# Optimization experiments

Hardware: AMD Instinct MI355X
Metric: run time of the kernel (lower is better)

Reference implementation:

```python
import jax, jax.numpy as jnp
import numpy as np

V, D, H, F, L, B, S = 32000, 1024, 16, 4096, 6, 2, 1024
DH = D // H


def setup_inputs() -> dict:
    key = jax.random.key(0)
    ks = jax.random.split(key, 12)
    n = lambda k, shape: jax.random.normal(k, shape, jnp.float32) * 0.02
    inp = {}
    inp['x'] = jax.random.randint(ks[0], (B, S), 0, V)
    # causal mask: 1 = masked (upper triangle), matches masked_fill(mask==1, -inf)
    inp['mask'] = jnp.triu(jnp.ones((S, S), jnp.int32), k=1)[None, None]
    inp['embed'] = n(ks[1], (V, D))
    inp['wq'] = n(ks[2], (L, D, D)); inp['bq'] = jnp.zeros((L, D), jnp.float32)
    inp['wk'] = n(ks[3], (L, D, D)); inp['bk'] = jnp.zeros((L, D), jnp.float32)
    inp['wv'] = n(ks[4], (L, D, D)); inp['bv'] = jnp.zeros((L, D), jnp.float32)
    inp['wo'] = n(ks[5], (L, D, D)); inp['bo'] = jnp.zeros((L, D), jnp.float32)
    inp['w1'] = n(ks[6], (L, D, F)); inp['b1'] = jnp.zeros((L, F), jnp.float32)
    inp['w2'] = n(ks[7], (L, F, D)); inp['b2'] = jnp.zeros((L, D), jnp.float32)
    inp['ln1_g'] = jnp.ones((L, D), jnp.float32); inp['ln1_b'] = jnp.zeros((L, D), jnp.float32)
    inp['ln2_g'] = jnp.ones((L, D), jnp.float32); inp['ln2_b'] = jnp.zeros((L, D), jnp.float32)
    inp['lnf_g'] = jnp.ones((D,), jnp.float32); inp['lnf_b'] = jnp.zeros((D,), jnp.float32)
    inp['proj_w'] = n(ks[8], (D, V)); inp['proj_b'] = jnp.zeros((V,), jnp.float32)
    return inp


def _layernorm(x, g, b, eps=1e-5):
    mu = jnp.mean(x, axis=-1, keepdims=True)
    var = jnp.var(x, axis=-1, keepdims=True)
    return (x - mu) * jax.lax.rsqrt(var + eps) * g + b


def _positional_encoding(s, d):
    pos = jnp.arange(s, dtype=jnp.float32)[:, None]
    div = jnp.exp(jnp.arange(0, d, 2, dtype=jnp.float32) * (-jnp.log(10000.0) / d))
    pe = jnp.zeros((s, d), jnp.float32)
    pe = pe.at[:, 0::2].set(jnp.sin(pos * div))
    pe = pe.at[:, 1::2].set(jnp.cos(pos * div))
    return pe


def reference(x, mask, embed, wq, bq, wk, bk, wv, bv, wo, bo, w1, b1, w2, b2,
              ln1_g, ln1_b, ln2_g, ln2_b, lnf_g, lnf_b, proj_w, proj_b):
    b_, s_ = x.shape
    h = embed[x] * jnp.sqrt(jnp.float32(D))          # [B,S,D]
    h = h + _positional_encoding(s_, D)[None]
    scale = 1.0 / jnp.sqrt(jnp.float32(DH))

    def layer(h, p):
        Wq, Bq, Wk, Bk, Wv, Bv, Wo, Bo, W1, B1, W2, B2, G1, Be1, G2, Be2 = p
        q = (h @ Wq + Bq).reshape(b_, s_, H, DH).transpose(0, 2, 1, 3)   # [B,H,S,Dh]
        k = (h @ Wk + Bk).reshape(b_, s_, H, DH).transpose(0, 2, 1, 3)
        v = (h @ Wv + Bv).reshape(b_, s_, H, DH).transpose(0, 2, 1, 3)
        scores = jnp.einsum('bhqd,bhkd->bhqk', q, k) * scale            # [B,H,S,S]
        scores = jnp.where(mask == 1, -jnp.inf, scores)
        attn = jax.nn.softmax(scores, axis=-1)
        ctx = jnp.einsum('bhqk,bhkd->bhqd', attn, v)
        ctx = ctx.transpose(0, 2, 1, 3).reshape(b_, s_, D) @ Wo + Bo
        h = _layernorm(h + ctx, G1, Be1)
        ffn = jax.nn.relu(h @ W1 + B1) @ W2 + B2
        h = _layernorm(h + ffn, G2, Be2)
        return h, None

    h, _ = jax.lax.scan(layer, h, (wq, bq, wk, bk, wv, bv, wo, bo,
                                   w1, b1, w2, b2, ln1_g, ln1_b, ln2_g, ln2_b))
    h = _layernorm(h, lnf_g, lnf_b)
    return h @ proj_w + proj_b                                           # [B,S,V]
```

## Files before the change

kernel.cpp:

```cpp
#include <hip/hip_runtime.h>
#include <math.h>

#define D_MODEL 1024
#define NHEADS 16
#define DHEAD 64
#define FDIM 4096
#define NLAYERS 6
#define BATCH 2
#define SEQ 1024
#define NROWS (BATCH*SEQ)
#define VOCAB 32000

typedef __attribute__((ext_vector_type(4))) float f32x4;
typedef __attribute__((ext_vector_type(4))) __bf16 bf16x4;
typedef __attribute__((ext_vector_type(8))) __bf16 bf16x8;

__device__ __forceinline__ void gll16(const void* g, void* l) {
  __builtin_amdgcn_global_load_lds(
      (const __attribute__((address_space(1))) unsigned int*)g,
      (__attribute__((address_space(3))) unsigned int*)l, 16, 0, 0);
}

__global__ __launch_bounds__(256) void transpose_w(
    const float* __restrict__ W, __bf16* __restrict__ Wt, int K, int N) {
  __shared__ __bf16 Ls[64][68];
  const size_t moff = (size_t)blockIdx.z * K * N;
  const float* Wl = W + moff;
  __bf16* Wtl = Wt + moff;
  const int n0 = blockIdx.x * 64, k0 = blockIdx.y * 64;
  const int tid = threadIdx.x;
  #pragma unroll
  for (int p = 0; p < 4; ++p) {
    int e = tid + p * 256;
    int r = e >> 4, c4 = (e & 15) * 4;
    float4 v = *(const float4*)&Wl[(size_t)(k0 + r) * N + n0 + c4];
    Ls[c4 + 0][r] = (__bf16)v.x; Ls[c4 + 1][r] = (__bf16)v.y;
    Ls[c4 + 2][r] = (__bf16)v.z; Ls[c4 + 3][r] = (__bf16)v.w;
  }
  __syncthreads();
  #pragma unroll
  for (int p = 0; p < 4; ++p) {
    int e = tid + p * 256;
    int r2 = e >> 4, c8 = (e & 15) * 4;
    bf16x4 o{Ls[r2][c8], Ls[r2][c8 + 1], Ls[r2][c8 + 2], Ls[r2][c8 + 3]};
    *(bf16x4*)&Wtl[(size_t)(n0 + r2) * K + k0 + c8] = o;
  }
}

struct GemmP {
  const __bf16* A;
  const __bf16* W[3];
  const float* B[3];
  void* C[3];
  int N, K;
};

template<int BM, int RELU, int OUTF32>
__global__ __launch_bounds__(256) void gemm_bf16(GemmP g) {
  constexpr int BK = 64;
  const __bf16* __restrict__ A = g.A;
  const __bf16* __restrict__ W = g.W[blockIdx.z];
  const float* __restrict__ bias = g.B[blockIdx.z];
  const int N = g.N, K = g.K;

  __shared__ __bf16 As[2][BM * BK];
  __shared__ __bf16 Bs[2][128 * BK];

  const int tid = threadIdx.x;
  const int lane = tid & 63, w = tid >> 6;

  const int gx = gridDim.x;
  const int nblk = gx * gridDim.y;
  const int id = blockIdx.x + blockIdx.y * gx;
  const int per = nblk >> 3;
  const int sid = (id & 7) * per + (id >> 3);
  const int row0 = (sid % gx) * BM;
  const int col0 = (sid / gx) * 128;

  const int wm = w >> 1, wn = w & 1;
  const int lr = lane & 15, rsw = lr & 7;

  constexpr int MI = BM / 32;
  f32x4 acc[MI][4] = {};

  const int swg = ((lane & 7) ^ (lane >> 3)) * 8;
  const __bf16* Ag = A + (size_t)(row0 + w * (BM / 4) + (lane >> 3)) * K + swg;
  const __bf16* Wg = W + (size_t)(col0 + w * 32 + (lane >> 3)) * K + swg;

  const int NT = K / BK;

  auto stage = [&](int buf, int t) {
    const int k0 = t * BK;
    #pragma unroll
    for (int s = 0; s < BM / 32; ++s)
      gll16(Ag + (size_t)s * 8 * K + k0, &As[buf][(w * (BM / 4) + s * 8) * BK]);
    #pragma unroll
    for (int s = 0; s < 4; ++s)
      gll16(Wg + (size_t)s * 8 * K + k0, &Bs[buf][(w * 32 + s * 8) * BK]);
  };

  stage(0, 0);
  __syncthreads();

  int cur = 0;
  for (int t = 0; t < NT; ++t) {
    if (t + 1 < NT) stage(cur ^ 1, t + 1);
    #pragma unroll
    for (int kk = 0; kk < 2; ++kk) {
      const int gsw = ((kk * 4 + (lane >> 4)) ^ rsw) * 8;
      bf16x8 af[MI], bf[4];
      #pragma unroll
      for (int i = 0; i < MI; ++i)
        af[i] = *(const bf16x8*)&As[cur][(wm * (BM / 2) + i * 16 + lr) * BK + gsw];
      #pragma unroll
      for (int j = 0; j < 4; ++j)
        bf[j] = *(const bf16x8*)&Bs[cur][(wn * 64 + j * 16 + lr) * BK + gsw];
      #pragma unroll
      for (int i = 0; i < MI; ++i)
        #pragma unroll
        for (int j = 0; j < 4; ++j)
          acc[i][j] = __builtin_amdgcn_mfma_f32_16x16x32_bf16(af[i], bf[j], acc[i][j], 0, 0, 0);
    }
    __syncthreads();
    cur ^= 1;
  }

  #pragma unroll
  for (int i = 0; i < MI; ++i) {
    #pragma unroll
    for (int j = 0; j < 4; ++j) {
      int col = col0 + wn * 64 + j * 16 + lr;
      float bb = bias[col];
      #pragma unroll
      for (int r = 0; r < 4; ++r) {
        int row = row0 + wm * (BM / 2) + i * 16 + (lane >> 4) * 4 + r;
        float v = acc[i][j][r] + bb;
        if (RELU) v = fmaxf(v, 0.0f);
        if (OUTF32) ((float*)g.C[blockIdx.z])[(size_t)row * N + col] = v;
        else ((__bf16*)g.C[blockIdx.z])[(size_t)row * N + col] = (__bf16)v;
      }
    }
  }
}

__global__ __launch_bounds__(512, 1) void gemm_256(
    const __bf16* __restrict__ A, const __bf16* __restrict__ W,
    const float* __restrict__ bias, float* __restrict__ C, int N, int K) {
  extern __shared__ __bf16 sm[];
  __bf16* As = sm;
  __bf16* Bs = sm + 2 * 256 * 64;

  const int tid = threadIdx.x;
  const int lane = tid & 63, w = tid >> 6;

  const int gx = gridDim.x;
  const int nblk = gx * gridDim.y;
  const int id = blockIdx.x + blockIdx.y * gx;
  const int per = nblk >> 3;
  const int sid = (id & 7) * per + (id >> 3);
  const int row0 = (sid % gx) * 256;
  const int col0 = (sid / gx) * 256;

  const int wr = w >> 2, wc = w & 3;
  const int lr = lane & 15;

  f32x4 acc[8][4] = {};

  const int swg = ((lane & 7) ^ (lane >> 3)) * 8;
  const __bf16* Ag = A + (size_t)(row0 + w * 32 + (lane >> 3)) * K + swg;
  const __bf16* Wg = W + (size_t)(col0 + w * 32 + (lane >> 3)) * K + swg;

  const int NT = K / 64;

  auto stage = [&](int buf, int t) {
    const int k0 = t * 64;
    #pragma unroll
    for (int s = 0; s < 4; ++s) {
      gll16(Ag + (size_t)(s * 8) * K + k0, &As[buf * 16384 + (w * 32 + s * 8) * 64]);
      gll16(Wg + (size_t)(s * 8) * K + k0, &Bs[buf * 16384 + (w * 32 + s * 8) * 64]);
    }
  };

  stage(0, 0);
  __syncthreads();

  int cur = 0;
  for (int t = 0; t < NT; ++t) {
    if (t + 1 < NT) stage(cur ^ 1, t + 1);
    #pragma unroll
    for (int kk = 0; kk < 2; ++kk) {
      bf16x8 af[8], bf[4];
      #pragma unroll
      for (int i = 0; i < 8; ++i) {
        int row = wr * 128 + i * 16 + lr;
        af[i] = *(const bf16x8*)&As[cur * 16384 + row * 64 +
                                    (((kk * 4 + (lane >> 4)) ^ (row & 7)) * 8)];
      }
      #pragma unroll
      for (int j = 0; j < 4; ++j) {
        int row = wc * 64 + j * 16 + lr;
        bf[j] = *(const bf16x8*)&Bs[cur * 16384 + row * 64 +
                                    (((kk * 4 + (lane >> 4)) ^ (row & 7)) * 8)];
      }
      #pragma unroll
      for (int i = 0; i < 8; ++i)
        #pragma unroll
        for (int j = 0; j < 4; ++j)
          acc[i][j] = __builtin_amdgcn_mfma_f32_16x16x32_bf16(af[i], bf[j], acc[i][j], 0, 0, 0);
    }
    __syncthreads();
    cur ^= 1;
  }

  #pragma unroll
  for (int i = 0; i < 8; ++i) {
    #pragma unroll
    for (int j = 0; j < 4; ++j) {
      int col = col0 + wc * 64 + j * 16 + lr;
      float bb = bias[col];
      #pragma unroll
      for (int r = 0; r < 4; ++r) {
        int row = row0 + wr * 128 + i * 16 + (lane >> 4) * 4 + r;
        C[(size_t)row * N + col] = acc[i][j][r] + bb;
      }
    }
  }
}

__global__ __launch_bounds__(256) void attn_kernel(
    const __bf16* __restrict__ Q, const __bf16* __restrict__ K,
    const __bf16* __restrict__ V, __bf16* __restrict__ O) {
  __shared__ __bf16 Ks[64 * 64];
  __shared__ __bf16 Vts[64 * 64];
  __shared__ __bf16 Psm[4][16 * 64];

  const int tid = threadIdx.x;
  const int lane = tid & 63, w = tid >> 6;
  const int q0 = blockIdx.x * 64;
  const int bh = blockIdx.y;
  const int b = bh >> 4, h = bh & 15;
  const size_t base = ((size_t)b * SEQ) * D_MODEL + (size_t)h * DHEAD;

  const int lr = lane & 15;
  const int lk = (lane >> 4) * 8;

  bf16x8 qa[2];
  {
    const __bf16* qp = Q + base + (size_t)(q0 + w * 16 + lr) * D_MODEL;
    qa[0] = *(const bf16x8*)&qp[lk];
    qa[1] = *(const bf16x8*)&qp[32 + lk];
  }

  f32x4 o_acc[4] = {};
  float m[4], l[4];
  #pragma unroll
  for (int r = 0; r < 4; ++r) { m[r] = -1e30f; l[r] = 0.0f; }

  const int nck = q0 / 64 + 1;

  for (int ck = 0; ck < nck; ++ck) {
    const int kv0 = ck * 64;
    __syncthreads();
    #pragma unroll
    for (int c = 0; c < 2; ++c) {
      int e = tid + c * 256;
      int r = e >> 3, d8 = (e & 7) * 8;
      const size_t grow = base + (size_t)(kv0 + r) * D_MODEL + d8;
      bf16x8 kv = *(const bf16x8*)&K[grow];
      *(bf16x8*)&Ks[(r * 64 + d8) ^ ((r & 7) << 3)] = kv;
      bf16x8 vv = *(const bf16x8*)&V[grow];
      #pragma unroll
      for (int j = 0; j < 8; ++j)
        Vts[((d8 + j) * 64 + r) ^ (((d8 + j) & 7) << 3)] = vv[j];
    }
    __syncthreads();

    f32x4 s_acc[4] = {};
    #pragma unroll
    for (int t = 0; t < 4; ++t) {
      int row = t * 16 + lr;
      #pragma unroll
      for (int hh = 0; hh < 2; ++hh) {
        bf16x8 kb = *(const bf16x8*)&Ks[(row * 64 + hh * 32 + lk) ^ ((row & 7) << 3)];
        s_acc[t] = __builtin_amdgcn_mfma_f32_16x16x32_bf16(qa[hh], kb, s_acc[t], 0, 0, 0);
      }
    }

    const bool diag = (ck == nck - 1);
    #pragma unroll
    for (int t = 0; t < 4; ++t) {
      int kvg = kv0 + t * 16 + lr;
      #pragma unroll
      for (int r = 0; r < 4; ++r) {
        float sv = s_acc[t][r] * 0.125f;
        if (diag) {
          int qg = q0 + w * 16 + (lane >> 4) * 4 + r;
          if (kvg > qg) sv = -1e30f;
        }
        s_acc[t][r] = sv;
      }
    }

    #pragma unroll
    for (int r = 0; r < 4; ++r) {
      float cm = fmaxf(fmaxf(s_acc[0][r], s_acc[1][r]), fmaxf(s_acc[2][r], s_acc[3][r]));
      #pragma unroll
      for (int off = 1; off < 16; off <<= 1) cm = fmaxf(cm, __shfl_xor(cm, off, 64));
      float newm = fmaxf(m[r], cm);
      float sc = __expf(m[r] - newm);
      m[r] = newm;
      float psum = 0.0f;
      #pragma unroll
      for (int t = 0; t < 4; ++t) {
        float p = __expf(s_acc[t][r] - newm);
        s_acc[t][r] = p;
        psum += p;
      }
      #pragma unroll
      for (int off = 1; off < 16; off <<= 1) psum += __shfl_xor(psum, off, 64);
      l[r] = l[r] * sc + psum;
      #pragma unroll
      for (int t = 0; t < 4; ++t) o_acc[t][r] *= sc;
    }

    #pragma unroll
    for (int t = 0; t < 4; ++t) {
      #pragma unroll
      for (int r = 0; r < 4; ++r) {
        int ql = (lane >> 4) * 4 + r;
        Psm[w][(ql * 64 + t * 16 + lr) ^ ((ql & 7) << 3)] = (__bf16)(s_acc[t][r]);
      }
    }

    bf16x8 pa[2];
    #pragma unroll
    for (int hh = 0; hh < 2; ++hh)
      pa[hh] = *(const bf16x8*)&Psm[w][(lr * 64 + hh * 32 + lk) ^ ((lr & 7) << 3)];
    #pragma unroll
    for (int t = 0; t < 4; ++t) {
      int row = t * 16 + lr;
      #pragma unroll
      for (int hh = 0; hh < 2; ++hh) {
        bf16x8 vb = *(const bf16x8*)&Vts[(row * 64 + hh * 32 + lk) ^ ((row & 7) << 3)];
        o_acc[t] = __builtin_amdgcn_mfma_f32_16x16x32_bf16(pa[hh], vb, o_acc[t], 0, 0, 0);
      }
    }
  }

  #pragma unroll
  for (int r = 0; r < 4; ++r) {
    float inv = 1.0f / l[r];
    int qg = q0 + w * 16 + (lane >> 4) * 4 + r;
    #pragma unroll
    for (int t = 0; t < 4; ++t)
      O[base + (size_t)qg * D_MODEL + t * 16 + lr] = (__bf16)(o_acc[t][r] * inv);
  }
}

template<int HASRES>
__global__ __launch_bounds__(256) void addln_kernel(
    const __bf16* __restrict__ X, const __bf16* __restrict__ Rr,
    const float* __restrict__ g, const float* __restrict__ bb,
    __bf16* __restrict__ Out) {
  const int row = blockIdx.x;
  const int tid = threadIdx.x;
  const size_t rb = (size_t)row * D_MODEL + tid * 4;
  bf16x4 xv = *(const bf16x4*)&X[rb];
  float v[4];
  float s = 0.0f, ss = 0.0f;
  if (HASRES) {
    bf16x4 rv = *(const bf16x4*)&Rr[rb];
    #pragma unroll
    for (int i = 0; i < 4; ++i) {
      v[i] = (float)xv[i] + (float)rv[i];
      s += v[i]; ss += v[i] * v[i];
    }
  } else {
    #pragma unroll
    for (int i = 0; i < 4; ++i) { v[i] = (float)xv[i]; s += v[i]; ss += v[i] * v[i]; }
  }
  #pragma unroll
  for (int off = 32; off; off >>= 1) { s += __shfl_xor(s, off, 64); ss += __shfl_xor(ss, off, 64); }
  __shared__ float red[8];
  const int lane = tid & 63, w = tid >> 6;
  if (lane == 0) { red[w] = s; red[4 + w] = ss; }
  __syncthreads();
  s = red[0] + red[1] + red[2] + red[3];
  ss = red[4] + red[5] + red[6] + red[7];
  float mean = s * (1.0f / D_MODEL);
  float var = ss * (1.0f / D_MODEL) - mean * mean;
  float rs = rsqrtf(var + 1e-5f);
  const int d0 = tid * 4;
  bf16x4 ov;
  #pragma unroll
  for (int i = 0; i < 4; ++i)
    ov[i] = (__bf16)((v[i] - mean) * rs * g[d0 + i] + bb[d0 + i]);
  *(bf16x4*)&Out[rb] = ov;
}

__global__ __launch_bounds__(256) void embed_kernel(
    const int* __restrict__ x, const float* __restrict__ embed,
    __bf16* __restrict__ H) {
  const int row = blockIdx.x;
  const int spos = row & (SEQ - 1);
  const int tok = x[row];
  const int tid = threadIdx.x;
  const int d0 = tid * 4;
  float4 e4 = *(const float4*)&embed[(size_t)tok * D_MODEL + d0];
  float ev[4] = {e4.x, e4.y, e4.z, e4.w};
  bf16x4 ov;
  #pragma unroll
  for (int i = 0; i < 4; ++i) {
    int d = d0 + i;
    float div = expf((float)(2 * (d >> 1)) * (-9.2103403719761836f / (float)D_MODEL));
    float ang = (float)spos * div;
    float pe = (d & 1) ? cosf(ang) : sinf(ang);
    ov[i] = (__bf16)(ev[i] * 32.0f + pe);
  }
  *(bf16x4*)&H[(size_t)row * D_MODEL + d0] = ov;
}

extern "C" void kernel_launch(void* const* d_in, const int* in_sizes, int n_in,
                              void* d_out, int out_size, void* d_ws, size_t ws_size,
                              hipStream_t stream) {
  const int* x = (const int*)d_in[0];
  const float* embed = (const float*)d_in[2];
  const float* wq = (const float*)d_in[3];
  const float* bq = (const float*)d_in[4];
  const float* wk = (const float*)d_in[5];
  const float* bk = (const float*)d_in[6];
  const float* wv = (const float*)d_in[7];
  const float* bv = (const float*)d_in[8];
  const float* wo = (const float*)d_in[9];
  const float* bo = (const float*)d_in[10];
  const float* w1 = (const float*)d_in[11];
  const float* b1 = (const float*)d_in[12];
  const float* w2 = (const float*)d_in[13];
  const float* b2 = (const float*)d_in[14];
  const float* ln1g = (const float*)d_in[15];
  const float* ln1b = (const float*)d_in[16];
  const float* ln2g = (const float*)d_in[17];
  const float* ln2b = (const float*)d_in[18];
  const float* lnfg = (const float*)d_in[19];
  const float* lnfb = (const float*)d_in[20];
  const float* pw = (const float*)d_in[21];
  const float* pb = (const float*)d_in[22];
  float* out = (float*)d_out;

  char* wsp = (char*)d_ws;
  size_t off = 0;
  auto alloc = [&](size_t bytes) {
    void* p = wsp + off; off = (off + bytes + 255) & ~(size_t)255; return p;
  };
  const size_t RD2 = (size_t)NROWS * D_MODEL * 2;
  __bf16* Xb   = (__bf16*)alloc(RD2);
  __bf16* Qb   = (__bf16*)alloc(RD2);
  __bf16* Kb   = (__bf16*)alloc(RD2);
  __bf16* Vb   = (__bf16*)alloc(RD2);
  __bf16* CTXb = (__bf16*)alloc(RD2);
  __bf16* Tb   = (__bf16*)alloc(RD2);
  __bf16* H1b  = (__bf16*)alloc(RD2);
  __bf16* FFb  = Qb;
  const size_t DD = (size_t)D_MODEL * D_MODEL;
  const size_t DF = (size_t)D_MODEL * FDIM;
  __bf16* wqt = (__bf16*)alloc(NLAYERS * DD * 2);
  __bf16* wkt = (__bf16*)alloc(NLAYERS * DD * 2);
  __bf16* wvt = (__bf16*)alloc(NLAYERS * DD * 2);
  __bf16* wot = (__bf16*)alloc(NLAYERS * DD * 2);
  __bf16* w1t = (__bf16*)alloc(NLAYERS * DF * 2);
  __bf16* w2t = (__bf16*)alloc(NLAYERS * DF * 2);
  __bf16* pwt = (__bf16*)alloc((size_t)D_MODEL * VOCAB * 2);

  transpose_w<<<dim3(16, 16, NLAYERS), 256, 0, stream>>>(wq, wqt, D_MODEL, D_MODEL);
  transpose_w<<<dim3(16, 16, NLAYERS), 256, 0, stream>>>(wk, wkt, D_MODEL, D_MODEL);
  transpose_w<<<dim3(16, 16, NLAYERS), 256, 0, stream>>>(wv, wvt, D_MODEL, D_MODEL);
  transpose_w<<<dim3(16, 16, NLAYERS), 256, 0, stream>>>(wo, wot, D_MODEL, D_MODEL);
  transpose_w<<<dim3(64, 16, NLAYERS), 256, 0, stream>>>(w1, w1t, D_MODEL, FDIM);
  transpose_w<<<dim3(16, 64, NLAYERS), 256, 0, stream>>>(w2, w2t, FDIM, D_MODEL);
  transpose_w<<<dim3(500, 16, 1), 256, 0, stream>>>(pw, pwt, D_MODEL, VOCAB);

  embed_kernel<<<NROWS, 256, 0, stream>>>(x, embed, Xb);

  for (int l = 0; l < NLAYERS; ++l) {
    GemmP g{};
    g.A = Xb; g.N = D_MODEL; g.K = D_MODEL;
    g.W[0] = wqt + l * DD; g.W[1] = wkt + l * DD; g.W[2] = wvt + l * DD;
    g.B[0] = bq + l * D_MODEL; g.B[1] = bk + l * D_MODEL; g.B[2] = bv + l * D_MODEL;
    g.C[0] = Qb; g.C[1] = Kb; g.C[2] = Vb;
    gemm_bf16<128, 0, 0><<<dim3(NROWS / 128, D_MODEL / 128, 3), 256, 0, stream>>>(g);

    attn_kernel<<<dim3(SEQ / 64, BATCH * NHEADS), 256, 0, stream>>>(Qb, Kb, Vb, CTXb);

    GemmP go{};
    go.A = CTXb; go.N = D_MODEL; go.K = D_MODEL;
    go.W[0] = wot + l * DD; go.B[0] = bo + l * D_MODEL; go.C[0] = Tb;
    gemm_bf16<64, 0, 0><<<dim3(NROWS / 64, D_MODEL / 128, 1), 256, 0, stream>>>(go);

    addln_kernel<1><<<NROWS, 256, 0, stream>>>(Xb, Tb, ln1g + l * D_MODEL, ln1b + l * D_MODEL, H1b);

    GemmP g1{};
    g1.A = H1b; g1.N = FDIM; g1.K = D_MODEL;
    g1.W[0] = w1t + l * DF; g1.B[0] = b1 + l * FDIM; g1.C[0] = FFb;
    gemm_bf16<128, 1, 0><<<dim3(NROWS / 128, FDIM / 128, 1), 256, 0, stream>>>(g1);

    GemmP g2{};
    g2.A = FFb; g2.N = D_MODEL; g2.K = FDIM;
    g2.W[0] = w2t + l * DF; g2.B[0] = b2 + l * D_MODEL; g2.C[0] = Tb;
    gemm_bf16<64, 0, 0><<<dim3(NROWS / 64, D_MODEL / 128, 1), 256, 0, stream>>>(g2);

    addln_kernel<1><<<NROWS, 256, 0, stream>>>(H1b, Tb, ln2g + l * D_MODEL, ln2b + l * D_MODEL, Xb);
  }

  addln_kernel<0><<<NROWS, 256, 0, stream>>>(Xb, nullptr, lnfg, lnfb, H1b);

  static int lds_attr_set = 0;
  if (!lds_attr_set) {
    hipFuncSetAttribute((const void*)gemm_256,
                        hipFuncAttributeMaxDynamicSharedMemorySize, 131072);
    lds_attr_set = 1;
  }
  gemm_256<<<dim3(NROWS / 256, VOCAB / 256), 512, 131072, stream>>>(
      H1b, pwt, pb, out, VOCAB, D_MODEL);
}
```

Baseline: 1.511 ms.

## Pipeline vocab projection GEMM with fine-grained quarter-tile loads and barriers

Restructures the 256x256 output-projection GEMM so that global-to-LDS loads are issued in quarter-tile chunks interleaved with the MFMA phases of the current tile. It uses explicit vmcnt waits and s_barrier/s_setprio in place of a full __syncthreads per K-tile. The aim is to hide load latency and keep matrix cores busy. It also changes launch_bounds to 2 blocks per CU, though 128KB of LDS per block likely prevents co-residency. This adds register pressure and more barriers, and there is a risk of ordering bugs in the wait counts.

```diff
diff --git a/kernel.cpp b/kernel.cpp
--- a/kernel.cpp
+++ b/kernel.cpp
@@ -143,12 +143,12 @@
   }
 }
 
-__global__ __launch_bounds__(512, 1) void gemm_256(
+__global__ __launch_bounds__(512, 2) void gemm_256(
     const __bf16* __restrict__ A, const __bf16* __restrict__ W,
     const float* __restrict__ bias, float* __restrict__ C, int N, int K) {
   extern __shared__ __bf16 sm[];
-  __bf16* As = sm;
-  __bf16* Bs = sm + 2 * 256 * 64;
+  __bf16* Asm = sm;
+  __bf16* Bsm = sm + 2 * 256 * 64;
 
   const int tid = threadIdx.x;
   const int lane = tid & 63, w = tid >> 6;
@@ -167,49 +167,70 @@
   f32x4 acc[8][4] = {};
 
   const int swg = ((lane & 7) ^ (lane >> 3)) * 8;
-  const __bf16* Ag = A + (size_t)(row0 + w * 32 + (lane >> 3)) * K + swg;
-  const __bf16* Wg = W + (size_t)(col0 + w * 32 + (lane >> 3)) * K + swg;
+  const __bf16* Agb = A + (size_t)(row0 + (lane >> 3)) * K + swg;
+  const __bf16* Wgb = W + (size_t)(col0 + (lane >> 3)) * K + swg;
 
   const int NT = K / 64;
 
-  auto stage = [&](int buf, int t) {
-    const int k0 = t * 64;
-    #pragma unroll
-    for (int s = 0; s < 4; ++s) {
-      gll16(Ag + (size_t)(s * 8) * K + k0, &As[buf * 16384 + (w * 32 + s * 8) * 64]);
-      gll16(Wg + (size_t)(s * 8) * K + k0, &Bs[buf * 16384 + (w * 32 + s * 8) * 64]);
-    }
+  auto stage_half = [&](int idx) {
+    const int tile = idx >> 2, half = idx & 3;
+    const int buf = tile & 1;
+    const int k0 = tile * 64;
+    const int rowbase = (half & 1) * 128 + w * 16;
+    const __bf16* src = (half < 2 ? Wgb : Agb) + (size_t)rowbase * K + k0;
+    __bf16* dst = (half < 2 ? Bsm : Asm) + buf * 16384 + rowbase * 64;
+    gll16(src, dst);
+    gll16(src + (size_t)8 * K, dst + 8 * 64);
   };
 
-  stage(0, 0);
-  __syncthreads();
-
-  int cur = 0;
+  #pragma unroll
+  for (int i = 0; i < 5; ++i) stage_half(i);
+  asm volatile("s_waitcnt vmcnt(2)" ::: "memory");
+  __builtin_amdgcn_s_barrier();
+
   for (int t = 0; t < NT; ++t) {
-    if (t + 1 < NT) stage(cur ^ 1, t + 1);
-    #pragma unroll
-    for (int kk = 0; kk < 2; ++kk) {
-      bf16x8 af[8], bf[4];
-      #pragma unroll
-      for (int i = 0; i < 8; ++i) {
-        int row = wr * 128 + i * 16 + lr;
-        af[i] = *(const bf16x8*)&As[cur * 16384 + row * 64 +
-                                    (((kk * 4 + (lane >> 4)) ^ (row & 7)) * 8)];
-      }
-      #pragma unroll
-      for (int j = 0; j < 4; ++j) {
-        int row = wc * 64 + j * 16 + lr;
-        bf[j] = *(const bf16x8*)&Bs[cur * 16384 + row * 64 +
-                                    (((kk * 4 + (lane >> 4)) ^ (row & 7)) * 8)];
-      }
-      #pragma unroll
-      for (int i = 0; i < 8; ++i)
+    const int cur = t & 1;
+    bf16x8 bfr[4][2];
+    #pragma unroll
+    for (int h = 0; h < 4; ++h) {
+      if (h == 0) {
         #pragma unroll
-        for (int j = 0; j < 4; ++j)
-          acc[i][j] = __builtin_amdgcn_mfma_f32_16x16x32_bf16(af[i], bf[j], acc[i][j], 0, 0, 0);
-    }
-    __syncthreads();
-    cur ^= 1;
+        for (int j = 0; j < 4; ++j) {
+          int row = wc * 64 + j * 16 + lr;
+          #pragma unroll
+          for (int kk = 0; kk < 2; ++kk)
+            bfr[j][kk] = *(const bf16x8*)&Bsm[cur * 16384 + row * 64 +
+                                              (((kk * 4 + (lane >> 4)) ^ (row & 7)) * 8)];
+        }
+      }
+      bf16x8 afr[2][2];
+      #pragma unroll
+      for (int ii = 0; ii < 2; ++ii) {
+        int row = wr * 128 + (2 * h + ii) * 16 + lr;
+        #pragma unroll
+        for (int kk = 0; kk < 2; ++kk)
+          afr[ii][kk] = *(const bf16x8*)&Asm[cur * 16384 + row * 64 +
+                                             (((kk * 4 + (lane >> 4)) ^ (row & 7)) * 8)];
+      }
+      const int sidx = 4 * t + h + 5;
+      if (sidx < 4 * NT) stage_half(sidx);
+      if (h == 3) {
+        if (t + 2 < NT) asm volatile("s_waitcnt vmcnt(2)" ::: "memory");
+        else if (t + 1 < NT) asm volatile("s_waitcnt vmcnt(0)" ::: "memory");
+      }
+      __builtin_amdgcn_s_barrier();
+      __builtin_amdgcn_s_setprio(1);
+      #pragma unroll
+      for (int kk = 0; kk < 2; ++kk)
+        #pragma unroll
+        for (int ii = 0; ii < 2; ++ii)
+          #pragma unroll
+          for (int j = 0; j < 4; ++j)
+            acc[2 * h + ii][j] = __builtin_amdgcn_mfma_f32_16x16x32_bf16(
+                afr[ii][kk], bfr[j][kk], acc[2 * h + ii][j], 0, 0, 0);
+      __builtin_amdgcn_s_setprio(0);
+      __builtin_amdgcn_s_barrier();
+    }
   }
 
   #pragma unroll
@@ -513,12 +534,8 @@
 
   addln_kernel<0><<<NROWS, 256, 0, stream>>>(Xb, nullptr, lnfg, lnfb, H1b);
 
-  static int lds_attr_set = 0;
-  if (!lds_attr_set) {
-    hipFuncSetAttribute((const void*)gemm_256,
-                        hipFuncAttributeMaxDynamicSharedMemorySize, 131072);
-    lds_attr_set = 1;
-  }
+  hipFuncSetAttribute((const void*)gemm_256,
+                      hipFuncAttributeMaxDynamicSharedMemorySize, 131072);
   gemm_256<<<dim3(NROWS / 256, VOCAB / 256), 512, 131072, stream>>>(
       H1b, pwt, pb, out, VOCAB, D_MODEL);
 }
```

Result: no change. 1.510 ms (-0.0%).
